# Kernel tuning notes

Measured on AMD Instinct MI355X. Metric: run time of the kernel, lower is better.

The kernel has to match this reference:

```python
import jax, jax.numpy as jnp
import numpy as np

N_NODES = 50000
N_EDGES = 25000
NNZ = 600000
D = 128
H = 256
DEPTH = 2


def setup_inputs() -> dict:
    key = jax.random.key(0)
    ks = jax.random.split(key, 12)
    x = jax.random.normal(ks[0], (N_NODES, D), dtype=jnp.float32)
    v_idx = jax.random.randint(ks[1], (NNZ,), 0, N_NODES)
    e_idx = jax.random.randint(ks[2], (NNZ,), 0, N_EDGES)
    s = 0.05
    W1 = jax.random.normal(ks[3], (H, D), dtype=jnp.float32) * s
    b1 = jnp.zeros((H,), jnp.float32)
    W2 = jax.random.normal(ks[4], (D, H), dtype=jnp.float32) * s
    b2 = jnp.zeros((D,), jnp.float32)
    Wu = jax.random.normal(ks[5], (D, D), dtype=jnp.float32) * s
    bu = jnp.zeros((D,), jnp.float32)
    Wa = jax.random.normal(ks[6], (4, D), dtype=jnp.float32) * s
    ba = jnp.zeros((4,), jnp.float32)
    return {"x": x, "v_idx": v_idx, "e_idx": e_idx, "W1": W1, "b1": b1,
            "W2": W2, "b2": b2, "Wu": Wu, "bu": bu, "Wa": Wa, "ba": ba}


def reference(x, v_idx, e_idx, W1, b1, W2, b2, Wu, bu, Wa, ba):
    ones = jnp.ones((v_idx.shape[0],), x.dtype)
    # degrees for mean aggregation (clamped to avoid div-by-zero)
    edeg = jnp.maximum(jax.ops.segment_sum(ones, e_idx, num_segments=N_EDGES), 1.0)
    vdeg = jnp.maximum(jax.ops.segment_sum(ones, v_idx, num_segments=N_NODES), 1.0)

    def v2v_mean(m):
        # vertex -> hyperedge (mean), then hyperedge -> vertex (mean)
        e_feat = jax.ops.segment_sum(m[v_idx], e_idx, num_segments=N_EDGES) / edeg[:, None]
        return jax.ops.segment_sum(e_feat[e_idx], v_idx, num_segments=N_NODES) / vdeg[:, None]

    def update(h):
        m = jax.nn.relu(h @ W1.T + b1)   # [N, H]
        m = jax.nn.relu(m @ W2.T + b2)   # [N, D]  (dropout = identity in eval)
        m_i = v2v_mean(m)                # [N, D]
        return jax.nn.relu(h @ Wu.T + bu + m_i)

    for _ in range(DEPTH):
        x = update(x)
    a = x @ Wa.T + ba                    # [N, 4]
    return jax.nn.log_softmax(a, axis=1)
```

## Files before the change

### kernel.cpp

```cpp
#include <hip/hip_runtime.h>
#include <hip/hip_bf16.h>
#include <math.h>

#define N_NODES 50000
#define N_EDGES 25000
#define NNZ     600000
#define D       128
#define H       256

#define BW    98
#define NBE   256
#define NBV   511
#define CAPE  3072
#define CAPV  1536
#define CHUNK 4096

typedef short short8 __attribute__((ext_vector_type(8)));
typedef float floatx4 __attribute__((ext_vector_type(4)));

__device__ inline ushort f2bf(float f) {
    uint u = __float_as_uint(f);
    u += 0x7FFF + ((u >> 16) & 1);
    return (ushort)(u >> 16);
}
__device__ inline float bflo(uint u) { return __uint_as_float(u << 16); }
__device__ inline float bfhi(uint u) { return __uint_as_float(u & 0xffff0000u); }

__global__ void f32_to_bf16_vec(const float* __restrict__ src, ushort* __restrict__ dst, int n4) {
    int i = blockIdx.x * blockDim.x + threadIdx.x;
    if (i < n4) {
        float4 v = ((const float4*)src)[i];
        ushort4 o;
        o.x = f2bf(v.x); o.y = f2bf(v.y); o.z = f2bf(v.z); o.w = f2bf(v.w);
        ((ushort4*)dst)[i] = o;
    }
}

__global__ void bucket_place(const int* __restrict__ v_idx, const int* __restrict__ e_idx,
                             int* __restrict__ cntE, int* __restrict__ cntV,
                             int2* __restrict__ recE, int2* __restrict__ recV) {
    __shared__ int hE[NBE], hV[NBV];
    __shared__ int rE[NBE], rV[NBV];
    for (int i = threadIdx.x; i < NBE; i += 256) hE[i] = 0;
    for (int i = threadIdx.x; i < NBV; i += 256) hV[i] = 0;
    __syncthreads();
    int base = blockIdx.x * CHUNK;
    int end  = min(base + CHUNK, NNZ);
    int myE[16], myV[16];
    #pragma unroll
    for (int j = 0; j < 16; ++j) {
        int i = base + threadIdx.x + j * 256;
        myE[j] = -1; myV[j] = -1;
        if (i < end) {
            myE[j] = e_idx[i];
            myV[j] = v_idx[i];
            atomicAdd(&hE[myE[j] / BW], 1);
            atomicAdd(&hV[myV[j] / BW], 1);
        }
    }
    __syncthreads();
    for (int i = threadIdx.x; i < NBE; i += 256) {
        int c = hE[i];
        rE[i] = c ? atomicAdd(&cntE[i], c) : 0;
    }
    for (int i = threadIdx.x; i < NBV; i += 256) {
        int c = hV[i];
        rV[i] = c ? atomicAdd(&cntV[i], c) : 0;
    }
    __syncthreads();
    for (int i = threadIdx.x; i < NBE; i += 256) hE[i] = 0;
    for (int i = threadIdx.x; i < NBV; i += 256) hV[i] = 0;
    __syncthreads();
    #pragma unroll
    for (int j = 0; j < 16; ++j) {
        if (myE[j] >= 0) {
            int bk = myE[j] / BW;
            int p = rE[bk] + atomicAdd(&hE[bk], 1);
            recE[(size_t)bk * CAPE + p] = make_int2(myE[j], myV[j]);
            bk = myV[j] / BW;
            p = rV[bk] + atomicAdd(&hV[bk], 1);
            recV[(size_t)bk * CAPV + p] = make_int2(myV[j], myE[j]);
        }
    }
}

__global__ void bucket_final(const int2* __restrict__ recE, const int* __restrict__ cntE,
                             const int2* __restrict__ recV, const int* __restrict__ cntV,
                             int2* __restrict__ e_sd, float* __restrict__ erecip, int* __restrict__ e_vert,
                             int2* __restrict__ v_sd, float* __restrict__ vrecip, int* __restrict__ v_edge) {
    __shared__ int hist[BW], scn[BW], cur[BW];
    const bool eSide = blockIdx.x < NBE;
    const int b = eSide ? blockIdx.x : blockIdx.x - NBE;
    const int cap   = eSide ? CAPE : CAPV;
    const int2* rec = (eSide ? recE : recV) + (size_t)b * cap;
    const int cnt   = (eSide ? cntE : cntV)[b];
    const int nseg  = eSide ? N_EDGES : N_NODES;
    int2* sd        = eSide ? e_sd : v_sd;
    float* recip    = eSide ? erecip : vrecip;
    int* outv       = (eSide ? e_vert : v_edge) + (size_t)b * cap;
    const int k0 = b * BW;

    for (int i = threadIdx.x; i < BW; i += 256) hist[i] = 0;
    __syncthreads();
    for (int i = threadIdx.x; i < cnt; i += 256)
        atomicAdd(&hist[rec[i].x - k0], 1);
    __syncthreads();

    if (threadIdx.x < 64) {
        int lane = threadIdx.x;
        int v0 = hist[lane];
        int a = v0;
        #pragma unroll
        for (int d = 1; d < 64; d <<= 1) {
            int u = __shfl_up(a, d, 64);
            if (lane >= d) a += u;
        }
        scn[lane] = a - v0;
        int tot0 = __shfl(a, 63, 64);
        int v1 = (lane < BW - 64) ? hist[64 + lane] : 0;
        int a1 = v1;
        #pragma unroll
        for (int d = 1; d < 64; d <<= 1) {
            int u = __shfl_up(a1, d, 64);
            if (lane >= d) a1 += u;
        }
        if (lane < BW - 64) scn[64 + lane] = tot0 + a1 - v1;
    }
    __syncthreads();

    const int gbase = b * cap;
    for (int i = threadIdx.x; i < BW; i += 256) {
        int seg = k0 + i;
        if (seg < nseg) {
            sd[seg] = make_int2(gbase + scn[i], hist[i]);
            recip[seg] = 1.0f / (float)max(hist[i], 1);
        }
        cur[i] = scn[i];
    }
    __syncthreads();
    for (int i = threadIdx.x; i < cnt; i += 256) {
        int2 r = rec[i];
        int p = atomicAdd(&cur[r.x - k0], 1);
        outv[p] = r.y;
    }
}

#define LOADC(pp, t0, t1, t2, t3)                                                  \
    do {                                                                           \
        int j0  = list[(pp) + 0],  j1  = list[(pp) + 1];                           \
        int j2  = list[(pp) + 2],  j3  = list[(pp) + 3];                           \
        int j4  = list[(pp) + 4],  j5  = list[(pp) + 5];                           \
        int j6  = list[(pp) + 6],  j7  = list[(pp) + 7];                           \
        int j8  = list[(pp) + 8],  j9  = list[(pp) + 9];                           \
        int j10 = list[(pp) + 10], j11 = list[(pp) + 11];                          \
        int j12 = list[(pp) + 12], j13 = list[(pp) + 13];                          \
        int j14 = list[(pp) + 14], j15 = list[(pp) + 15];                          \
        int r0 = (q < 2) ? (q == 0 ? j0  : j1)  : (q == 2 ? j2  : j3);             \
        int r1 = (q < 2) ? (q == 0 ? j4  : j5)  : (q == 2 ? j6  : j7);             \
        int r2 = (q < 2) ? (q == 0 ? j8  : j9)  : (q == 2 ? j10 : j11);            \
        int r3 = (q < 2) ? (q == 0 ? j12 : j13) : (q == 2 ? j14 : j15);            \
        t0 = *(const uint4*)(sp + (size_t)r0 * D);                                 \
        t1 = *(const uint4*)(sp + (size_t)r1 * D);                                 \
        t2 = *(const uint4*)(sp + (size_t)r2 * D);                                 \
        t3 = *(const uint4*)(sp + (size_t)r3 * D);                                 \
    } while (0)

#define ACCC(t0, t1, t2, t3)                                                       \
    do {                                                                           \
        a0 += bflo(t0.x) + bflo(t1.x) + bflo(t2.x) + bflo(t3.x);                   \
        a1 += bfhi(t0.x) + bfhi(t1.x) + bfhi(t2.x) + bfhi(t3.x);                   \
        a2 += bflo(t0.y) + bflo(t1.y) + bflo(t2.y) + bflo(t3.y);                   \
        a3 += bfhi(t0.y) + bfhi(t1.y) + bfhi(t2.y) + bfhi(t3.y);                   \
        a4 += bflo(t0.z) + bflo(t1.z) + bflo(t2.z) + bflo(t3.z);                   \
        a5 += bfhi(t0.z) + bfhi(t1.z) + bfhi(t2.z) + bfhi(t3.z);                   \
        a6 += bflo(t0.w) + bflo(t1.w) + bflo(t2.w) + bflo(t3.w);                   \
        a7 += bfhi(t0.w) + bfhi(t1.w) + bfhi(t2.w) + bfhi(t3.w);                   \
    } while (0)

__global__ void gather_rows(const ushort* __restrict__ src,
                            const int2* __restrict__ sd,
                            const int* __restrict__ list,
                            const float* __restrict__ recip,
                            const ushort* __restrict__ uadd,
                            ushort* __restrict__ outbuf,
                            const float* __restrict__ Wa,
                            const float* __restrict__ ba,
                            float* __restrict__ headout,
                            int nseg) {
    int seg  = (int)(((long long)blockIdx.x * blockDim.x + threadIdx.x) >> 6);
    int lane = threadIdx.x & 63;
    if (seg >= nseg) return;
    const int q  = lane >> 4;
    const int ql = lane & 15;
    int2 dsc = sd[seg];
    int s   = __builtin_amdgcn_readfirstlane(dsc.x);
    int cnt = __builtin_amdgcn_readfirstlane(dsc.y);
    int e = s + cnt;
    const ushort* sp = src + ql * 8;

    float a0 = 0.f, a1 = 0.f, a2 = 0.f, a3 = 0.f;
    float a4 = 0.f, a5 = 0.f, a6 = 0.f, a7 = 0.f;

    int p = s;
    if (p + 16 <= e) {
        uint4 t0, t1, t2, t3;
        LOADC(p, t0, t1, t2, t3);
        p += 16;
        while (p + 16 <= e) {
            uint4 n0, n1, n2, n3;
            LOADC(p, n0, n1, n2, n3);
            ACCC(t0, t1, t2, t3);
            t0 = n0; t1 = n1; t2 = n2; t3 = n3;
            p += 16;
        }
        ACCC(t0, t1, t2, t3);
    }
    for (; p + 4 <= e; p += 4) {
        int i0 = list[p + 0], i1 = list[p + 1], i2 = list[p + 2], i3 = list[p + 3];
        int r0 = (q < 2) ? (q == 0 ? i0 : i1) : (q == 2 ? i2 : i3);
        uint4 t0 = *(const uint4*)(sp + (size_t)r0 * D);
        a0 += bflo(t0.x);  a1 += bfhi(t0.x);
        a2 += bflo(t0.y);  a3 += bfhi(t0.y);
        a4 += bflo(t0.z);  a5 += bfhi(t0.z);
        a6 += bflo(t0.w);  a7 += bfhi(t0.w);
    }
    if (p < e) {
        int rem = e - p;
        if (q < rem) {
            int r0 = list[p + q];
            uint4 t0 = *(const uint4*)(sp + (size_t)r0 * D);
            a0 += bflo(t0.x);  a1 += bfhi(t0.x);
            a2 += bflo(t0.y);  a3 += bfhi(t0.y);
            a4 += bflo(t0.z);  a5 += bfhi(t0.z);
            a6 += bflo(t0.w);  a7 += bfhi(t0.w);
        }
    }

    a0 += __shfl_xor(a0, 16, 64); a0 += __shfl_xor(a0, 32, 64);
    a1 += __shfl_xor(a1, 16, 64); a1 += __shfl_xor(a1, 32, 64);
    a2 += __shfl_xor(a2, 16, 64); a2 += __shfl_xor(a2, 32, 64);
    a3 += __shfl_xor(a3, 16, 64); a3 += __shfl_xor(a3, 32, 64);
    a4 += __shfl_xor(a4, 16, 64); a4 += __shfl_xor(a4, 32, 64);
    a5 += __shfl_xor(a5, 16, 64); a5 += __shfl_xor(a5, 32, 64);
    a6 += __shfl_xor(a6, 16, 64); a6 += __shfl_xor(a6, 32, 64);
    a7 += __shfl_xor(a7, 16, 64); a7 += __shfl_xor(a7, 32, 64);

    if (q == 0) {
        float rc = recip[seg];
        float f0 = a0 * rc, f1 = a1 * rc, f2 = a2 * rc, f3 = a3 * rc;
        float f4 = a4 * rc, f5 = a5 * rc, f6 = a6 * rc, f7 = a7 * rc;
        if (uadd) {
            uint4 uv = *(const uint4*)(uadd + (size_t)seg * D + ql * 8);
            f0 = fmaxf(f0 + bflo(uv.x), 0.f);  f1 = fmaxf(f1 + bfhi(uv.x), 0.f);
            f2 = fmaxf(f2 + bflo(uv.y), 0.f);  f3 = fmaxf(f3 + bfhi(uv.y), 0.f);
            f4 = fmaxf(f4 + bflo(uv.z), 0.f);  f5 = fmaxf(f5 + bfhi(uv.z), 0.f);
            f6 = fmaxf(f6 + bflo(uv.w), 0.f);  f7 = fmaxf(f7 + bfhi(uv.w), 0.f);
        }
        if (headout) {
            float av[4];
            #pragma unroll
            for (int j = 0; j < 4; ++j) {
                const float* wr = Wa + j * D + ql * 8;
                float4 wA = *(const float4*)wr;
                float4 wB = *(const float4*)(wr + 4);
                float pj = f0 * wA.x + f1 * wA.y + f2 * wA.z + f3 * wA.w
                         + f4 * wB.x + f5 * wB.y + f6 * wB.z + f7 * wB.w;
                pj += __shfl_xor(pj, 1, 64);
                pj += __shfl_xor(pj, 2, 64);
                pj += __shfl_xor(pj, 4, 64);
                pj += __shfl_xor(pj, 8, 64);
                av[j] = pj + ba[j];
            }
            if (ql == 0) {
                float mx = fmaxf(fmaxf(av[0], av[1]), fmaxf(av[2], av[3]));
                float se = expf(av[0] - mx) + expf(av[1] - mx)
                         + expf(av[2] - mx) + expf(av[3] - mx);
                float lse = mx + logf(se);
                float4 o = make_float4(av[0] - lse, av[1] - lse, av[2] - lse, av[3] - lse);
                *(float4*)(headout + (size_t)seg * 4) = o;
            }
        } else {
            uint4 o;
            o.x = ((uint)f2bf(f1) << 16) | (uint)f2bf(f0);
            o.y = ((uint)f2bf(f3) << 16) | (uint)f2bf(f2);
            o.z = ((uint)f2bf(f5) << 16) | (uint)f2bf(f4);
            o.w = ((uint)f2bf(f7) << 16) | (uint)f2bf(f6);
            *(uint4*)(outbuf + (size_t)seg * D + ql * 8) = o;
        }
    }
}

__launch_bounds__(256, 3)
__global__ void mlp_fused(const ushort* __restrict__ A,
                          const ushort* __restrict__ W1b,
                          const float* __restrict__ b1,
                          const ushort* __restrict__ W2b,
                          const float* __restrict__ b2,
                          const ushort* __restrict__ Wub,
                          const float* __restrict__ bu,
                          ushort* __restrict__ m2out,
                          ushort* __restrict__ uout,
                          int M) {
    __shared__ ushort Af[64][136];
    __shared__ __align__(16) char Pbuf[18432];
    __shared__ ushort m1c[64][72];
    ushort* P = (ushort*)Pbuf;
    float (*Cs)[68] = (float(*)[68])Pbuf;

    const int tid = threadIdx.x;
    const int w = tid >> 6, lane = tid & 63;
    const int quad = lane >> 4, mrow = lane & 15;
    const int rowBase = blockIdx.x * 64;
    const int orow = tid >> 2;
    const int c0   = (tid & 3) << 4;

    #pragma unroll
    for (int r = 0; r < 4; ++r) {
        int idx = tid + r * 256;
        int row = idx >> 4;
        int c   = (idx & 15) << 3;
        uint4 av = make_uint4(0, 0, 0, 0);
        if (rowBase + row < M)
            av = *(const uint4*)(A + (size_t)(rowBase + row) * D + c);
        *(uint4*)&Af[row][c] = av;
    }

    for (int n0 = 0; n0 < D; n0 += 64) {
        __syncthreads();
        #pragma unroll
        for (int r = 0; r < 4; ++r) {
            int idx = tid + r * 256;
            int row = idx >> 4;
            int c   = (idx & 15) << 3;
            *(uint4*)&P[row * 136 + c] = *(const uint4*)(Wub + (size_t)(n0 + row) * D + c);
        }
        __syncthreads();
        floatx4 acc[4] = {{0,0,0,0},{0,0,0,0},{0,0,0,0},{0,0,0,0}};
        #pragma unroll
        for (int k0 = 0; k0 < D; k0 += 32) {
            short8 af = *(const short8*)&Af[w * 16 + mrow][k0 + quad * 8];
            #pragma unroll
            for (int t = 0; t < 4; ++t) {
                short8 bfr = *(const short8*)&P[(t * 16 + mrow) * 136 + k0 + quad * 8];
                acc[t] = __builtin_amdgcn_mfma_f32_16x16x32_bf16(af, bfr, acc[t], 0, 0, 0);
            }
        }
        __syncthreads();
        #pragma unroll
        for (int t = 0; t < 4; ++t)
            #pragma unroll
            for (int r = 0; r < 4; ++r)
                Cs[w * 16 + quad * 4 + r][t * 16 + mrow] = acc[t][r];
        __syncthreads();
        if (rowBase + orow < M) {
            union { ushort u16[16]; uint4 u4[2]; } ov;
            #pragma unroll
            for (int j4 = 0; j4 < 4; ++j4) {
                float4 bb = *(const float4*)(bu + n0 + c0 + j4 * 4);
                float bjv[4] = {bb.x, bb.y, bb.z, bb.w};
                #pragma unroll
                for (int j = 0; j < 4; ++j)
                    ov.u16[j4 * 4 + j] = f2bf(Cs[orow][c0 + j4 * 4 + j] + bjv[j]);
            }
            ushort* cp = uout + (size_t)(rowBase + orow) * D + n0 + c0;
            *(uint4*)cp = ov.u4[0];
            *(uint4*)(cp + 8) = ov.u4[1];
        }
    }

    floatx4 acc2[8] = {{0,0,0,0},{0,0,0,0},{0,0,0,0},{0,0,0,0},
                       {0,0,0,0},{0,0,0,0},{0,0,0,0},{0,0,0,0}};
    for (int kc = 0; kc < 4; ++kc) {
        __syncthreads();
        #pragma unroll
        for (int r = 0; r < 4; ++r) {
            int idx = tid + r * 256;
            int row = idx >> 4;
            int c   = (idx & 15) << 3;
            *(uint4*)&P[row * 136 + c] = *(const uint4*)(W1b + (size_t)(kc * 64 + row) * D + c);
        }
        __syncthreads();
        floatx4 acc1[4] = {{0,0,0,0},{0,0,0,0},{0,0,0,0},{0,0,0,0}};
        #pragma unroll
        for (int k0 = 0; k0 < D; k0 += 32) {
            short8 af = *(const short8*)&Af[w * 16 + mrow][k0 + quad * 8];
            #pragma unroll
            for (int t = 0; t < 4; ++t) {
                short8 bfr = *(const short8*)&P[(t * 16 + mrow) * 136 + k0 + quad * 8];
                acc1[t] = __builtin_amdgcn_mfma_f32_16x16x32_bf16(af, bfr, acc1[t], 0, 0, 0);
            }
        }
        #pragma unroll
        for (int t = 0; t < 4; ++t) {
            float bb = b1[kc * 64 + t * 16 + mrow];
            #pragma unroll
            for (int r = 0; r < 4; ++r)
                m1c[w * 16 + quad * 4 + r][t * 16 + mrow] = f2bf(fmaxf(acc1[t][r] + bb, 0.f));
        }
        __syncthreads();
        #pragma unroll
        for (int r = 0; r < 4; ++r) {
            int idx = tid + r * 256;
            int row = idx >> 3;
            int c8  = (idx & 7) << 3;
            *(uint4*)&P[row * 72 + c8] = *(const uint4*)(W2b + (size_t)row * H + kc * 64 + c8);
        }
        __syncthreads();
        #pragma unroll
        for (int k0 = 0; k0 < 64; k0 += 32) {
            short8 af = *(const short8*)&m1c[w * 16 + mrow][k0 + quad * 8];
            #pragma unroll
            for (int t2 = 0; t2 < 8; ++t2) {
                short8 bfr = *(const short8*)&P[(t2 * 16 + mrow) * 72 + k0 + quad * 8];
                acc2[t2] = __builtin_amdgcn_mfma_f32_16x16x32_bf16(af, bfr, acc2[t2], 0, 0, 0);
            }
        }
    }

    #pragma unroll
    for (int hh = 0; hh < 2; ++hh) {
        __syncthreads();
        #pragma unroll
        for (int t = 0; t < 4; ++t)
            #pragma unroll
            for (int r = 0; r < 4; ++r)
                Cs[w * 16 + quad * 4 + r][t * 16 + mrow] = acc2[hh * 4 + t][r];
        __syncthreads();
        if (rowBase + orow < M) {
            union { ushort u16[16]; uint4 u4[2]; } ov;
            #pragma unroll
            for (int j4 = 0; j4 < 4; ++j4) {
                float4 bb = *(const float4*)(b2 + hh * 64 + c0 + j4 * 4);
                float bjv[4] = {bb.x, bb.y, bb.z, bb.w};
                #pragma unroll
                for (int j = 0; j < 4; ++j) {
                    float v = Cs[orow][c0 + j4 * 4 + j] + bjv[j];
                    ov.u16[j4 * 4 + j] = f2bf(fmaxf(v, 0.f));
                }
            }
            ushort* cp = m2out + (size_t)(rowBase + orow) * D + hh * 64 + c0;
            *(uint4*)cp = ov.u4[0];
            *(uint4*)(cp + 8) = ov.u4[1];
        }
    }
}

extern "C" void kernel_launch(void* const* d_in, const int* in_sizes, int n_in,
                              void* d_out, int out_size, void* d_ws, size_t ws_size,
                              hipStream_t stream) {
    const float* x     = (const float*)d_in[0];
    const int*   v_idx = (const int*)d_in[1];
    const int*   e_idx = (const int*)d_in[2];
    const float* W1    = (const float*)d_in[3];
    const float* b1    = (const float*)d_in[4];
    const float* W2    = (const float*)d_in[5];
    const float* b2    = (const float*)d_in[6];
    const float* Wu    = (const float*)d_in[7];
    const float* bu    = (const float*)d_in[8];
    const float* Wa    = (const float*)d_in[9];
    const float* ba    = (const float*)d_in[10];
    float* out = (float*)d_out;

    char* wsp = (char*)d_ws;
    auto alloc = [&](size_t bytes) -> char* {
        char* p = wsp;
        wsp += (bytes + 255) & ~(size_t)255;
        return p;
    };

    ushort* xb     = (ushort*)alloc((size_t)N_NODES * D * 2);
    ushort* hA     = (ushort*)alloc((size_t)N_NODES * D * 2);
    ushort* m2b    = (ushort*)alloc((size_t)N_NODES * D * 2);
    ushort* ub     = (ushort*)alloc((size_t)N_NODES * D * 2);
    ushort* e_feat = (ushort*)alloc((size_t)N_EDGES * D * 2);
    ushort* W1b    = (ushort*)alloc((size_t)H * D * 2);
    ushort* W2b    = (ushort*)alloc((size_t)D * H * 2);
    ushort* Wub    = (ushort*)alloc((size_t)D * D * 2);
    int*    e_vert = (int*)alloc((size_t)NBE * CAPE * 4);
    int*    v_edge = (int*)alloc((size_t)NBV * CAPV * 4);
    int2*   recE   = (int2*)alloc((size_t)NBE * CAPE * 8);
    int2*   recV   = (int2*)alloc((size_t)NBV * CAPV * 8);
    int*    cntE   = (int*)alloc((size_t)(NBE + NBV) * 4);
    int*    cntV   = cntE + NBE;
    int2*   e_sd   = (int2*)alloc((size_t)N_EDGES * 8);
    int2*   v_sd   = (int2*)alloc((size_t)N_NODES * 8);
    float*  erecip = (float*)alloc((size_t)N_EDGES * 4);
    float*  vrecip = (float*)alloc((size_t)N_NODES * 4);

    const int cooBlocks = (NNZ + CHUNK - 1) / CHUNK;

    f32_to_bf16_vec<<<(N_NODES * D / 4 + 255) / 256, 256, 0, stream>>>(x, xb, N_NODES * D / 4);
    f32_to_bf16_vec<<<(H * D / 4 + 255) / 256, 256, 0, stream>>>(W1, W1b, H * D / 4);
    f32_to_bf16_vec<<<(D * H / 4 + 255) / 256, 256, 0, stream>>>(W2, W2b, D * H / 4);
    f32_to_bf16_vec<<<(D * D / 4 + 255) / 256, 256, 0, stream>>>(Wu, Wub, D * D / 4);

    hipMemsetAsync(cntE, 0, (size_t)(NBE + NBV) * 4, stream);
    bucket_place<<<cooBlocks, 256, 0, stream>>>(v_idx, e_idx, cntE, cntV, recE, recV);
    bucket_final<<<NBE + NBV, 256, 0, stream>>>(recE, cntE, recV, cntV,
                                                e_sd, erecip, e_vert,
                                                v_sd, vrecip, v_edge);

    const int gridM = (N_NODES + 63) / 64;

    const ushort* h = xb;
    for (int depth = 0; depth < 2; ++depth) {
        mlp_fused<<<gridM, 256, 0, stream>>>(h, W1b, b1, W2b, b2, Wub, bu, m2b, ub, N_NODES);
        gather_rows<<<(N_EDGES * 64 + 255) / 256, 256, 0, stream>>>(
            m2b, e_sd, e_vert, erecip, nullptr, e_feat, nullptr, nullptr, nullptr, N_EDGES);
        if (depth == 0) {
            gather_rows<<<(N_NODES * 64 + 255) / 256, 256, 0, stream>>>(
                e_feat, v_sd, v_edge, vrecip, ub, hA, nullptr, nullptr, nullptr, N_NODES);
            h = hA;
        } else {
            gather_rows<<<(N_NODES * 64 + 255) / 256, 256, 0, stream>>>(
                e_feat, v_sd, v_edge, vrecip, ub, nullptr, Wa, ba, out, N_NODES);
        }
    }
}
```

Baseline: 298.5 us.

## Gather with 16 lanes per segment and merge bf16 conversion kernels

The gather kernel now assigns one 16-lane group per segment instead of a full 64-lane wavefront. Each lane loops over all of the segment's rows, loading four at a time, which removes the cross-quarter shuffle reduction and packs four segments into each wavefront. Separately, the four fp32-to-bf16 conversion launches are merged into a single kernel that picks its source by index range. In exchange, the gather loses its software prefetch pipeline and uniform scalar loop bounds, so segments of different lengths within one wavefront cause divergence and less memory-level parallelism per segment.

```diff
diff --git a/kernel.cpp b/kernel.cpp
--- a/kernel.cpp
+++ b/kernel.cpp
@@ -26,14 +26,25 @@
 __device__ inline float bflo(uint u) { return __uint_as_float(u << 16); }
 __device__ inline float bfhi(uint u) { return __uint_as_float(u & 0xffff0000u); }
 
-__global__ void f32_to_bf16_vec(const float* __restrict__ src, ushort* __restrict__ dst, int n4) {
+__global__ void convert_all(const float* __restrict__ x,  ushort* __restrict__ xb,
+                            const float* __restrict__ W1, ushort* __restrict__ W1b,
+                            const float* __restrict__ W2, ushort* __restrict__ W2b,
+                            const float* __restrict__ Wu, ushort* __restrict__ Wub) {
+    const int nx = N_NODES * D / 4;
+    const int n1 = H * D / 4;
+    const int n2 = D * H / 4;
+    const int nu = D * D / 4;
     int i = blockIdx.x * blockDim.x + threadIdx.x;
-    if (i < n4) {
-        float4 v = ((const float4*)src)[i];
-        ushort4 o;
-        o.x = f2bf(v.x); o.y = f2bf(v.y); o.z = f2bf(v.z); o.w = f2bf(v.w);
-        ((ushort4*)dst)[i] = o;
-    }
+    const float* src; ushort* dst; int j = i;
+    if (j < nx)                { src = x;  dst = xb;  }
+    else if ((j -= nx) < n1)   { src = W1; dst = W1b; }
+    else if ((j -= n1) < n2)   { src = W2; dst = W2b; }
+    else if ((j -= n2) < nu)   { src = Wu; dst = Wub; }
+    else return;
+    float4 v = ((const float4*)src)[j];
+    ushort4 o;
+    o.x = f2bf(v.x); o.y = f2bf(v.y); o.z = f2bf(v.z); o.w = f2bf(v.w);
+    ((ushort4*)dst)[j] = o;
 }
 
 __global__ void bucket_place(const int* __restrict__ v_idx, const int* __restrict__ e_idx,
@@ -145,38 +156,6 @@
     }
 }
 
-#define LOADC(pp, t0, t1, t2, t3)                                                  \
-    do {                                                                           \
-        int j0  = list[(pp) + 0],  j1  = list[(pp) + 1];                           \
-        int j2  = list[(pp) + 2],  j3  = list[(pp) + 3];                           \
-        int j4  = list[(pp) + 4],  j5  = list[(pp) + 5];                           \
-        int j6  = list[(pp) + 6],  j7  = list[(pp) + 7];                           \
-        int j8  = list[(pp) + 8],  j9  = list[(pp) + 9];                           \
-        int j10 = list[(pp) + 10], j11 = list[(pp) + 11];                          \
-        int j12 = list[(pp) + 12], j13 = list[(pp) + 13];                          \
-        int j14 = list[(pp) + 14], j15 = list[(pp) + 15];                          \
-        int r0 = (q < 2) ? (q == 0 ? j0  : j1)  : (q == 2 ? j2  : j3);             \
-        int r1 = (q < 2) ? (q == 0 ? j4  : j5)  : (q == 2 ? j6  : j7);             \
-        int r2 = (q < 2) ? (q == 0 ? j8  : j9)  : (q == 2 ? j10 : j11);            \
-        int r3 = (q < 2) ? (q == 0 ? j12 : j13) : (q == 2 ? j14 : j15);            \
-        t0 = *(const uint4*)(sp + (size_t)r0 * D);                                 \
-        t1 = *(const uint4*)(sp + (size_t)r1 * D);                                 \
-        t2 = *(const uint4*)(sp + (size_t)r2 * D);                                 \
-        t3 = *(const uint4*)(sp + (size_t)r3 * D);                                 \
-    } while (0)
-
-#define ACCC(t0, t1, t2, t3)                                                       \
-    do {                                                                           \
-        a0 += bflo(t0.x) + bflo(t1.x) + bflo(t2.x) + bflo(t3.x);                   \
-        a1 += bfhi(t0.x) + bfhi(t1.x) + bfhi(t2.x) + bfhi(t3.x);                   \
-        a2 += bflo(t0.y) + bflo(t1.y) + bflo(t2.y) + bflo(t3.y);                   \
-        a3 += bfhi(t0.y) + bfhi(t1.y) + bfhi(t2.y) + bfhi(t3.y);                   \
-        a4 += bflo(t0.z) + bflo(t1.z) + bflo(t2.z) + bflo(t3.z);                   \
-        a5 += bfhi(t0.z) + bfhi(t1.z) + bfhi(t2.z) + bfhi(t3.z);                   \
-        a6 += bflo(t0.w) + bflo(t1.w) + bflo(t2.w) + bflo(t3.w);                   \
-        a7 += bfhi(t0.w) + bfhi(t1.w) + bfhi(t2.w) + bfhi(t3.w);                   \
-    } while (0)
-
 __global__ void gather_rows(const ushort* __restrict__ src,
                             const int2* __restrict__ sd,
                             const int* __restrict__ list,
@@ -187,106 +166,85 @@
                             const float* __restrict__ ba,
                             float* __restrict__ headout,
                             int nseg) {
-    int seg  = (int)(((long long)blockIdx.x * blockDim.x + threadIdx.x) >> 6);
-    int lane = threadIdx.x & 63;
+    long long gtid = (long long)blockIdx.x * blockDim.x + threadIdx.x;
+    int seg = (int)(gtid >> 4);
+    int ql  = threadIdx.x & 15;
     if (seg >= nseg) return;
-    const int q  = lane >> 4;
-    const int ql = lane & 15;
     int2 dsc = sd[seg];
-    int s   = __builtin_amdgcn_readfirstlane(dsc.x);
-    int cnt = __builtin_amdgcn_readfirstlane(dsc.y);
-    int e = s + cnt;
+    int s = dsc.x, cnt = dsc.y;
     const ushort* sp = src + ql * 8;
 
-    float a0 = 0.f, a1 = 0.f, a2 = 0.f, a3 = 0.f;
-    float a4 = 0.f, a5 = 0.f, a6 = 0.f, a7 = 0.f;
-
-    int p = s;
-    if (p + 16 <= e) {
-        uint4 t0, t1, t2, t3;
-        LOADC(p, t0, t1, t2, t3);
-        p += 16;
-        while (p + 16 <= e) {
-            uint4 n0, n1, n2, n3;
-            LOADC(p, n0, n1, n2, n3);
-            ACCC(t0, t1, t2, t3);
-            t0 = n0; t1 = n1; t2 = n2; t3 = n3;
-            p += 16;
-        }
-        ACCC(t0, t1, t2, t3);
-    }
-    for (; p + 4 <= e; p += 4) {
-        int i0 = list[p + 0], i1 = list[p + 1], i2 = list[p + 2], i3 = list[p + 3];
-        int r0 = (q < 2) ? (q == 0 ? i0 : i1) : (q == 2 ? i2 : i3);
+    float f0 = 0.f, f1 = 0.f, f2 = 0.f, f3 = 0.f;
+    float f4 = 0.f, f5 = 0.f, f6 = 0.f, f7 = 0.f;
+
+    int p = 0;
+    for (; p + 4 <= cnt; p += 4) {
+        int r0 = list[s + p + 0];
+        int r1 = list[s + p + 1];
+        int r2 = list[s + p + 2];
+        int r3 = list[s + p + 3];
         uint4 t0 = *(const uint4*)(sp + (size_t)r0 * D);
-        a0 += bflo(t0.x);  a1 += bfhi(t0.x);
-        a2 += bflo(t0.y);  a3 += bfhi(t0.y);
-        a4 += bflo(t0.z);  a5 += bfhi(t0.z);
-        a6 += bflo(t0.w);  a7 += bfhi(t0.w);
-    }
-    if (p < e) {
-        int rem = e - p;
-        if (q < rem) {
-            int r0 = list[p + q];
-            uint4 t0 = *(const uint4*)(sp + (size_t)r0 * D);
-            a0 += bflo(t0.x);  a1 += bfhi(t0.x);
-            a2 += bflo(t0.y);  a3 += bfhi(t0.y);
-            a4 += bflo(t0.z);  a5 += bfhi(t0.z);
-            a6 += bflo(t0.w);  a7 += bfhi(t0.w);
-        }
-    }
-
-    a0 += __shfl_xor(a0, 16, 64); a0 += __shfl_xor(a0, 32, 64);
-    a1 += __shfl_xor(a1, 16, 64); a1 += __shfl_xor(a1, 32, 64);
-    a2 += __shfl_xor(a2, 16, 64); a2 += __shfl_xor(a2, 32, 64);
-    a3 += __shfl_xor(a3, 16, 64); a3 += __shfl_xor(a3, 32, 64);
-    a4 += __shfl_xor(a4, 16, 64); a4 += __shfl_xor(a4, 32, 64);
-    a5 += __shfl_xor(a5, 16, 64); a5 += __shfl_xor(a5, 32, 64);
-    a6 += __shfl_xor(a6, 16, 64); a6 += __shfl_xor(a6, 32, 64);
-    a7 += __shfl_xor(a7, 16, 64); a7 += __shfl_xor(a7, 32, 64);
-
-    if (q == 0) {
-        float rc = recip[seg];
-        float f0 = a0 * rc, f1 = a1 * rc, f2 = a2 * rc, f3 = a3 * rc;
-        float f4 = a4 * rc, f5 = a5 * rc, f6 = a6 * rc, f7 = a7 * rc;
-        if (uadd) {
-            uint4 uv = *(const uint4*)(uadd + (size_t)seg * D + ql * 8);
-            f0 = fmaxf(f0 + bflo(uv.x), 0.f);  f1 = fmaxf(f1 + bfhi(uv.x), 0.f);
-            f2 = fmaxf(f2 + bflo(uv.y), 0.f);  f3 = fmaxf(f3 + bfhi(uv.y), 0.f);
-            f4 = fmaxf(f4 + bflo(uv.z), 0.f);  f5 = fmaxf(f5 + bfhi(uv.z), 0.f);
-            f6 = fmaxf(f6 + bflo(uv.w), 0.f);  f7 = fmaxf(f7 + bfhi(uv.w), 0.f);
-        }
-        if (headout) {
-            float av[4];
-            #pragma unroll
-            for (int j = 0; j < 4; ++j) {
-                const float* wr = Wa + j * D + ql * 8;
-                float4 wA = *(const float4*)wr;
-                float4 wB = *(const float4*)(wr + 4);
-                float pj = f0 * wA.x + f1 * wA.y + f2 * wA.z + f3 * wA.w
-                         + f4 * wB.x + f5 * wB.y + f6 * wB.z + f7 * wB.w;
-                pj += __shfl_xor(pj, 1, 64);
-                pj += __shfl_xor(pj, 2, 64);
-                pj += __shfl_xor(pj, 4, 64);
-                pj += __shfl_xor(pj, 8, 64);
-                av[j] = pj + ba[j];
-            }
-            if (ql == 0) {
-                float mx = fmaxf(fmaxf(av[0], av[1]), fmaxf(av[2], av[3]));
-                float se = expf(av[0] - mx) + expf(av[1] - mx)
-                         + expf(av[2] - mx) + expf(av[3] - mx);
-                float lse = mx + logf(se);
-                float4 o = make_float4(av[0] - lse, av[1] - lse, av[2] - lse, av[3] - lse);
-                *(float4*)(headout + (size_t)seg * 4) = o;
-            }
-        } else {
-            uint4 o;
-            o.x = ((uint)f2bf(f1) << 16) | (uint)f2bf(f0);
-            o.y = ((uint)f2bf(f3) << 16) | (uint)f2bf(f2);
-            o.z = ((uint)f2bf(f5) << 16) | (uint)f2bf(f4);
-            o.w = ((uint)f2bf(f7) << 16) | (uint)f2bf(f6);
-            *(uint4*)(outbuf + (size_t)seg * D + ql * 8) = o;
-        }
+        uint4 t1 = *(const uint4*)(sp + (size_t)r1 * D);
+        uint4 t2 = *(const uint4*)(sp + (size_t)r2 * D);
+        uint4 t3 = *(const uint4*)(sp + (size_t)r3 * D);
+        f0 += bflo(t0.x) + bflo(t1.x) + bflo(t2.x) + bflo(t3.x);
+        f1 += bfhi(t0.x) + bfhi(t1.x) + bfhi(t2.x) + bfhi(t3.x);
+        f2 += bflo(t0.y) + bflo(t1.y) + bflo(t2.y) + bflo(t3.y);
+        f3 += bfhi(t0.y) + bfhi(t1.y) + bfhi(t2.y) + bfhi(t3.y);
+        f4 += bflo(t0.z) + bflo(t1.z) + bflo(t2.z) + bflo(t3.z);
+        f5 += bfhi(t0.z) + bfhi(t1.z) + bfhi(t2.z) + bfhi(t3.z);
+        f6 += bflo(t0.w) + bflo(t1.w) + bflo(t2.w) + bflo(t3.w);
+        f7 += bfhi(t0.w) + bfhi(t1.w) + bfhi(t2.w) + bfhi(t3.w);
+    }
+    for (; p < cnt; ++p) {
+        int r0 = list[s + p];
+        uint4 t0 = *(const uint4*)(sp + (size_t)r0 * D);
+        f0 += bflo(t0.x);  f1 += bfhi(t0.x);
+        f2 += bflo(t0.y);  f3 += bfhi(t0.y);
+        f4 += bflo(t0.z);  f5 += bfhi(t0.z);
+        f6 += bflo(t0.w);  f7 += bfhi(t0.w);
+    }
+
+    float rc = recip[seg];
+    f0 *= rc; f1 *= rc; f2 *= rc; f3 *= rc;
+    f4 *= rc; f5 *= rc; f6 *= rc; f7 *= rc;
+    if (uadd) {
+        uint4 uv = *(const uint4*)(uadd + (size_t)seg * D + ql * 8);
+        f0 = fmaxf(f0 + bflo(uv.x), 0.f);  f1 = fmaxf(f1 + bfhi(uv.x), 0.f);
+        f2 = fmaxf(f2 + bflo(uv.y), 0.f);  f3 = fmaxf(f3 + bfhi(uv.y), 0.f);
+        f4 = fmaxf(f4 + bflo(uv.z), 0.f);  f5 = fmaxf(f5 + bfhi(uv.z), 0.f);
+        f6 = fmaxf(f6 + bflo(uv.w), 0.f);  f7 = fmaxf(f7 + bfhi(uv.w), 0.f);
+    }
+    if (headout) {
+        float av[4];
+        #pragma unroll
+        for (int j = 0; j < 4; ++j) {
+            const float* wr = Wa + j * D + ql * 8;
+            float4 wA = *(const float4*)wr;
+            float4 wB = *(const float4*)(wr + 4);
+            float pj = f0 * wA.x + f1 * wA.y + f2 * wA.z + f3 * wA.w
+                     + f4 * wB.x + f5 * wB.y + f6 * wB.z + f7 * wB.w;
+            pj += __shfl_xor(pj, 1, 64);
+            pj += __shfl_xor(pj, 2, 64);
+            pj += __shfl_xor(pj, 4, 64);
+            pj += __shfl_xor(pj, 8, 64);
+            av[j] = pj + ba[j];
+        }
+        if (ql == 0) {
+            float mx = fmaxf(fmaxf(av[0], av[1]), fmaxf(av[2], av[3]));
+            float se = expf(av[0] - mx) + expf(av[1] - mx)
+                     + expf(av[2] - mx) + expf(av[3] - mx);
+            float lse = mx + logf(se);
+            float4 o = make_float4(av[0] - lse, av[1] - lse, av[2] - lse, av[3] - lse);
+            *(float4*)(headout + (size_t)seg * 4) = o;
+        }
+    } else {
+        uint4 o;
+        o.x = ((uint)f2bf(f1) << 16) | (uint)f2bf(f0);
+        o.y = ((uint)f2bf(f3) << 16) | (uint)f2bf(f2);
+        o.z = ((uint)f2bf(f5) << 16) | (uint)f2bf(f4);
+        o.w = ((uint)f2bf(f7) << 16) | (uint)f2bf(f6);
+        *(uint4*)(outbuf + (size_t)seg * D + ql * 8) = o;
     }
 }
 
@@ -488,11 +446,10 @@
     float*  vrecip = (float*)alloc((size_t)N_NODES * 4);
 
     const int cooBlocks = (NNZ + CHUNK - 1) / CHUNK;
-
-    f32_to_bf16_vec<<<(N_NODES * D / 4 + 255) / 256, 256, 0, stream>>>(x, xb, N_NODES * D / 4);
-    f32_to_bf16_vec<<<(H * D / 4 + 255) / 256, 256, 0, stream>>>(W1, W1b, H * D / 4);
-    f32_to_bf16_vec<<<(D * H / 4 + 255) / 256, 256, 0, stream>>>(W2, W2b, D * H / 4);
-    f32_to_bf16_vec<<<(D * D / 4 + 255) / 256, 256, 0, stream>>>(Wu, Wub, D * D / 4);
+    const int convTotal = N_NODES * D / 4 + H * D / 4 + D * H / 4 + D * D / 4;
+
+    convert_all<<<(convTotal + 255) / 256, 256, 0, stream>>>(
+        x, xb, W1, W1b, W2, W2b, Wu, Wub);
 
     hipMemsetAsync(cntE, 0, (size_t)(NBE + NBV) * 4, stream);
     bucket_place<<<cooBlocks, 256, 0, stream>>>(v_idx, e_idx, cntE, cntV, recE, recV);
@@ -501,18 +458,20 @@
                                                 v_sd, vrecip, v_edge);
 
     const int gridM = (N_NODES + 63) / 64;
+    const int gEdge = (N_EDGES * 16 + 255) / 256;
+    const int gVert = (N_NODES * 16 + 255) / 256;
 
     const ushort* h = xb;
     for (int depth = 0; depth < 2; ++depth) {
         mlp_fused<<<gridM, 256, 0, stream>>>(h, W1b, b1, W2b, b2, Wub, bu, m2b, ub, N_NODES);
-        gather_rows<<<(N_EDGES * 64 + 255) / 256, 256, 0, stream>>>(
+        gather_rows<<<gEdge, 256, 0, stream>>>(
             m2b, e_sd, e_vert, erecip, nullptr, e_feat, nullptr, nullptr, nullptr, N_EDGES);
         if (depth == 0) {
-            gather_rows<<<(N_NODES * 64 + 255) / 256, 256, 0, stream>>>(
+            gather_rows<<<gVert, 256, 0, stream>>>(
                 e_feat, v_sd, v_edge, vrecip, ub, hA, nullptr, nullptr, nullptr, N_NODES);
             h = hA;
         } else {
-            gather_rows<<<(N_NODES * 64 + 255) / 256, 256, 0, stream>>>(
+            gather_rows<<<gVert, 256, 0, stream>>>(
                 e_feat, v_sd, v_edge, vrecip, ub, nullptr, Wa, ba, out, N_NODES);
         }
     }
```

Result: faster. 269.6 us (-9.7%).
